# Optimization experiments

Hardware: AMD Instinct MI355X
Metric: run time of the kernel (lower is better)

Reference implementation:

```python
import jax, jax.numpy as jnp
import numpy as np


def setup_inputs() -> dict:
    key = jax.random.key(0)
    kx, kw = jax.random.split(key)
    x = jax.random.normal(kx, (32, 2048, 256), dtype=jnp.float32)
    W = jax.random.normal(kw, (1024, 256), dtype=jnp.float32)  # codebook [K, D]
    return {"x": x, "W": W}


def reference(x, W):
    D = W.shape[1]
    flat = x.reshape(-1, D)  # [N, D]
    # Squared Euclidean distances [N, K]; argmin is identical to cdist argmin.
    d2 = (
        jnp.sum(flat * flat, axis=1, keepdims=True)
        - 2.0 * (flat @ W.T)
        + jnp.sum(W * W, axis=1)
    )
    idx = jnp.argmin(d2, axis=1)  # [N]
    quant = W[idx].reshape(x.shape)  # direct gather == one-hot @ W
    # Straight-through estimator
    quantized = x + jax.lax.stop_gradient(quant - x)
    e_latent = jnp.mean((jax.lax.stop_gradient(quantized) - x) ** 2)
    q_latent = jnp.mean((quantized - jax.lax.stop_gradient(x)) ** 2)
    commitment_cost = 0.25
    loss = q_latent + commitment_cost * e_latent
    return quantized, loss, idx[:, None]
```

## Files before the change

### kernel.cpp

```cpp
#include <hip/hip_runtime.h>


#define NROWS    65536
#define DDIM     256
#define KCODES   1024
#define DEXT     512
#define ND_TOTAL 16777216

typedef __attribute__((ext_vector_type(8))) short bf16x8;
typedef __attribute__((ext_vector_type(4))) float floatx4;

__device__ __forceinline__ unsigned short f2bf(float f) {
    unsigned int u = __float_as_uint(f);
    return (unsigned short)((u + 0x7FFFu + ((u >> 16) & 1u)) >> 16);
}
__device__ __forceinline__ float bf2f(unsigned short h) {
    return __uint_as_float((unsigned int)h << 16);
}
__device__ __forceinline__ void split4(float4 v, ushort4* hi, ushort4* lo) {
    unsigned short hx = f2bf(v.x), hy = f2bf(v.y), hz = f2bf(v.z), hw = f2bf(v.w);
    *hi = make_ushort4(hx, hy, hz, hw);
    *lo = make_ushort4(f2bf(v.x - bf2f(hx)), f2bf(v.y - bf2f(hy)),
                       f2bf(v.z - bf2f(hz)), f2bf(v.w - bf2f(hw)));
}
__device__ __forceinline__ void async_copy16(void* lds, const void* g) {
    __builtin_amdgcn_global_load_lds(
        (const __attribute__((address_space(1))) unsigned int*)g,
        (__attribute__((address_space(3))) unsigned int*)lds, 16, 0, 0);
}

__device__ __forceinline__ void merge2(float& v1, int& k1, float& v2, int& k2,
                                       float o1, int ok1, float o2, int ok2) {
    bool aw = (v1 < o1) || (v1 == o1 && k1 < ok1);
    float ca = aw ? v2 : v1; int kca = aw ? k2 : k1;
    float cb = aw ? o1 : o2; int kcb = aw ? ok1 : ok2;
    float nv1 = aw ? v1 : o1; int nk1 = aw ? k1 : ok1;
    bool cw = (ca < cb) || (ca == cb && kca < kcb);
    v1 = nv1; k1 = nk1;
    v2 = cw ? ca : cb; k2 = cw ? kca : kcb;
}

__global__ __launch_bounds__(256) void vq_prepw(
    const float* __restrict__ W, unsigned short* __restrict__ What,
    float* __restrict__ w2, float* __restrict__ w2m,
    float* __restrict__ lossws, unsigned* __restrict__ ticket)
{
    int k = blockIdx.x * 256 + threadIdx.x;
    if (k == 0) { lossws[0] = 0.0f; ticket[0] = 0u; }
    const float4* wr = (const float4*)(W + (size_t)k * DDIM);
    unsigned short* hrow = What + (size_t)k * DEXT;
    float s = 0.0f;
    for (int i = 0; i < 64; ++i) {
        float4 v = wr[i];
        s = fmaf(v.x, v.x, s); s = fmaf(v.y, v.y, s);
        s = fmaf(v.z, v.z, s); s = fmaf(v.w, v.w, s);
        ushort4 hv, lv;
        split4(v, &hv, &lv);
        *(ushort4*)(hrow + i * 4) = hv;
        *(ushort4*)(hrow + 256 + i * 4) = lv;
    }
    w2[k] = s;
    w2m[k] = s - 256.0f;
}

__global__ __launch_bounds__(256, 2) void vq_main(
    unsigned short* Xhat, const unsigned short* __restrict__ What,
    const float* __restrict__ x, const float* __restrict__ W,
    const float* __restrict__ w2, const float* __restrict__ w2m,
    float* qout, float* lossws, unsigned* ticket, float* loss_out, float* idx_out)
{
    __shared__ __align__(16) unsigned short smem[2 * 16384];
    __shared__ float Wm[KCODES];

    int*   rk1   = (int*)smem;
    int*   rk2   = rk1 + 256;
    int*   candk = rk2 + 256;
    float* resc  = (float*)(candk + 512);
    int*   fink  = (int*)(resc + 512);

    const int tid  = threadIdx.x;
    const int wave = tid >> 6, lane = tid & 63;
    const int quad = lane >> 4, l15 = lane & 15;
    const int wr = wave >> 1, wc = wave & 1;
    const int row0 = blockIdx.x * 128;

    #pragma unroll
    for (int t = 0; t < 4; ++t) Wm[t * 256 + tid] = w2m[t * 256 + tid];

    #pragma unroll 4
    for (int it = 0; it < 32; ++it) {
        int gid = it * 256 + tid;
        int row = gid >> 6, qq = gid & 63;
        float4 v = ((const float4*)(x + (size_t)(row0 + row) * DDIM))[qq];
        ushort4 hv, lv;
        split4(v, &hv, &lv);
        unsigned short* r = Xhat + (size_t)(row0 + row) * DEXT;
        *(ushort4*)(r + qq * 4) = hv;
        *(ushort4*)(r + 256 + qq * 4) = lv;
    }
    __syncthreads();

    float s1[16], s2[16];
    #pragma unroll
    for (int s = 0; s < 16; ++s) { s1[s] = 3.0e38f; s2[s] = 3.0e38f; }

    const int r0 = tid >> 2, p0 = tid & 3;
    const int psw = (p0 ^ ((r0 >> 1) & 3)) << 3;
    const int quadS8 = (quad ^ ((l15 >> 1) & 3)) << 3;
    const unsigned short* Abase = Xhat + (size_t)row0 * DEXT + (size_t)r0 * DEXT + psw;
    const unsigned short* Bbase = What + (size_t)r0 * DEXT + psw;

    auto STAGE = [&](int q) {
        const int ct = q >> 3, dc = (q & 7) << 5;
        unsigned short* L = smem + (q & 1) * 16384 + tid * 8;
        const unsigned short* An = Abase + dc;
        const unsigned short* Bn = Bbase + (size_t)ct * 128 * DEXT + dc;
        async_copy16(L,          An);
        async_copy16(L + 2048,   An + 64 * DEXT);
        async_copy16(L + 4096,   An + 256);
        async_copy16(L + 6144,   An + 64 * DEXT + 256);
        async_copy16(L + 8192,   Bn);
        async_copy16(L + 10240,  Bn + 64 * DEXT);
        async_copy16(L + 12288,  Bn + 256);
        async_copy16(L + 14336,  Bn + 64 * DEXT + 256);
    };

    STAGE(0);

    floatx4 acc[4][4];
    #pragma unroll
    for (int i = 0; i < 4; ++i)
        #pragma unroll
        for (int j = 0; j < 4; ++j) acc[i][j] = (floatx4){0.f, 0.f, 0.f, 0.f};

    #pragma unroll 1
    for (int q = 0; q < 64; ++q) {
        asm volatile("s_waitcnt vmcnt(0)" ::: "memory");
        __builtin_amdgcn_s_barrier();
        asm volatile("" ::: "memory");
        if (q + 1 < 64) STAGE(q + 1);

        const unsigned short* Sb = smem + (q & 1) * 16384;
        bf16x8 a0[4], a1[4];
        #pragma unroll
        for (int i = 0; i < 4; ++i) {
            const int ro = (wr * 64 + i * 16 + l15) * 32 + quadS8;
            a0[i] = *(const bf16x8*)(Sb + ro);
            a1[i] = *(const bf16x8*)(Sb + 4096 + ro);
        }
        #pragma unroll
        for (int j = 0; j < 4; ++j) {
            const int ro = (wc * 64 + j * 16 + l15) * 32 + quadS8;
            bf16x8 b0 = *(const bf16x8*)(Sb + 8192 + ro);
            bf16x8 b1 = *(const bf16x8*)(Sb + 12288 + ro);
            __builtin_amdgcn_s_setprio(1);
            #pragma unroll
            for (int i = 0; i < 4; ++i) {
                acc[i][j] = __builtin_amdgcn_mfma_f32_16x16x32_bf16(a0[i], b0, acc[i][j], 0, 0, 0);
                acc[i][j] = __builtin_amdgcn_mfma_f32_16x16x32_bf16(a1[i], b1, acc[i][j], 0, 0, 0);
                acc[i][j] = __builtin_amdgcn_mfma_f32_16x16x32_bf16(a0[i], b1, acc[i][j], 0, 0, 0);
                acc[i][j] = __builtin_amdgcn_mfma_f32_16x16x32_bf16(a1[i], b0, acc[i][j], 0, 0, 0);
            }
            __builtin_amdgcn_s_setprio(0);
        }

        if ((q & 7) == 7) {
            const int ctf = q >> 3;
            #pragma unroll
            for (int j = 0; j < 4; ++j) {
                int cc = ctf * 128 + wc * 64 + j * 16 + l15;
                float wm = Wm[cc];
                unsigned pay = (unsigned)((j << 3) | ctf);
                #pragma unroll
                for (int i = 0; i < 4; ++i)
                    #pragma unroll
                    for (int r = 0; r < 4; ++r) {
                        float v = fmaf(-2.0f, acc[i][j][r], wm);
                        float pf = __uint_as_float((__float_as_uint(v) & 0xFFFFFFE0u) | pay);
                        int s = i * 4 + r;
                        float t = fminf(s1[s], pf);
                        s2[s] = fminf(s2[s], fmaxf(s1[s], pf));
                        s1[s] = t;
                    }
            }
            #pragma unroll
            for (int i = 0; i < 4; ++i)
                #pragma unroll
                for (int j = 0; j < 4; ++j) acc[i][j] = (floatx4){0.f, 0.f, 0.f, 0.f};
        }
    }

    float v1[16], v2[16];
    int k1[16], k2[16];
    #pragma unroll
    for (int s = 0; s < 16; ++s) {
        unsigned u1 = __float_as_uint(s1[s]) & 31u;
        unsigned u2 = __float_as_uint(s2[s]) & 31u;
        v1[s] = s1[s]; v2[s] = s2[s];
        k1[s] = (int)(u1 & 7u) * 128 + wc * 64 + (int)(u1 >> 3) * 16 + l15;
        k2[s] = (int)(u2 & 7u) * 128 + wc * 64 + (int)(u2 >> 3) * 16 + l15;
    }
    #pragma unroll
    for (int m = 1; m < 16; m <<= 1) {
        #pragma unroll
        for (int s = 0; s < 16; ++s) {
            float o1 = __shfl_xor(v1[s], m, 64);
            int  ok1 = __shfl_xor(k1[s], m, 64);
            float o2 = __shfl_xor(v2[s], m, 64);
            int  ok2 = __shfl_xor(k2[s], m, 64);
            merge2(v1[s], k1[s], v2[s], k2[s], o1, ok1, o2, ok2);
        }
    }
    if (l15 == 0) {
        #pragma unroll
        for (int s = 0; s < 16; ++s) {
            int row = wr * 64 + (s >> 2) * 16 + quad * 4 + (s & 3);
            rk1[wc * 128 + row] = k1[s];
            rk2[wc * 128 + row] = k2[s];
        }
    }
    __syncthreads();
    if (tid < 128) {
        candk[tid * 4 + 0] = rk1[tid];
        candk[tid * 4 + 1] = rk2[tid];
        candk[tid * 4 + 2] = rk1[128 + tid];
        candk[tid * 4 + 3] = rk2[128 + tid];
    }
    __syncthreads();
    #pragma unroll
    for (int j2 = 0; j2 < 2; ++j2) {
        int job = tid + j2 * 256;
        int r = job >> 2, cn = job & 3;
        int k = candk[r * 4 + cn];
        const float4* xr  = (const float4*)(x + (size_t)(row0 + r) * DDIM);
        const float4* wrp = (const float4*)(W + (size_t)k * DDIM);
        float dot = 0.0f;
        #pragma unroll 8
        for (int i = 0; i < 64; ++i) {
            float4 va = xr[i], vb = wrp[i];
            dot = fmaf(va.x, vb.x, dot); dot = fmaf(va.y, vb.y, dot);
            dot = fmaf(va.z, vb.z, dot); dot = fmaf(va.w, vb.w, dot);
        }
        resc[r * 4 + cn] = fmaf(-2.0f, dot, w2[k]);
    }
    __syncthreads();
    if (tid < 128) {
        float bd = resc[tid * 4 + 0];
        int   bk = candk[tid * 4 + 0];
        #pragma unroll
        for (int cn = 1; cn < 4; ++cn) {
            float d = resc[tid * 4 + cn];
            int   k = candk[tid * 4 + cn];
            if (d < bd || (d == bd && k < bk)) { bd = d; bk = k; }
        }
        fink[tid] = bk;
        idx_out[row0 + tid] = (float)bk;
    }
    __syncthreads();

    const int c4 = tid & 63, rsub = tid >> 6;
    float lsum = 0.0f;
    for (int it2 = 0; it2 < 32; ++it2) {
        int r = it2 * 4 + rsub;
        int k = fink[r];
        float4 wv = ((const float4*)(W + (size_t)k * DDIM))[c4];
        float4 xv = ((const float4*)(x + (size_t)(row0 + r) * DDIM))[c4];
        ((float4*)(qout + (size_t)(row0 + r) * DDIM))[c4] = wv;
        float dx = wv.x - xv.x, dy = wv.y - xv.y;
        float dz = wv.z - xv.z, dw = wv.w - xv.w;
        lsum = fmaf(dx, dx, lsum); lsum = fmaf(dy, dy, lsum);
        lsum = fmaf(dz, dz, lsum); lsum = fmaf(dw, dw, lsum);
    }
    #pragma unroll
    for (int off = 32; off > 0; off >>= 1) lsum += __shfl_down(lsum, off, 64);
    if (lane == 0) atomicAdd(lossws, lsum);

    __syncthreads();
    if (tid == 0) {
        __threadfence();
        unsigned old = atomicAdd(ticket, 1u);
        if (old == 511u) {
            float total = atomicAdd(lossws, 0.0f);
            loss_out[0] = 1.25f * total / (float)ND_TOTAL;
        }
    }
}

extern "C" void kernel_launch(void* const* d_in, const int* in_sizes, int n_in,
                              void* d_out, int out_size, void* d_ws, size_t ws_size,
                              hipStream_t stream) {
    const float* x = (const float*)d_in[0];
    const float* W = (const float*)d_in[1];
    float* out = (float*)d_out;
    unsigned short* Xhat = (unsigned short*)d_out;
    unsigned short* What = (unsigned short*)d_ws;
    float* w2     = (float*)((char*)d_ws + (1 << 20));
    float* w2m    = w2 + 1024;
    float* lossws = w2 + 2048;
    unsigned* ticket = (unsigned*)(w2 + 2049);
    float* loss_out = out + (size_t)ND_TOTAL;
    float* idx_out  = out + (size_t)ND_TOTAL + 1;

    vq_prepw<<<4, 256, 0, stream>>>(W, What, w2, w2m, lossws, ticket);
    vq_main<<<512, 256, 0, stream>>>(Xhat, What, x, W, w2, w2m, out,
                                     lossws, ticket, loss_out, idx_out);
}
```

Measured before the change: 335.7 us.

## Halve block row tile to 64, drop lo*lo MFMA term, rank top-4 candidates

```diff
diff --git a/kernel.cpp b/kernel.cpp
--- a/kernel.cpp
+++ b/kernel.cpp
@@ -63,32 +63,34 @@
     w2m[k] = s - 256.0f;
 }
 
-__global__ __launch_bounds__(256, 2) void vq_main(
+__global__ __launch_bounds__(256, 3) void vq_main(
     unsigned short* Xhat, const unsigned short* __restrict__ What,
     const float* __restrict__ x, const float* __restrict__ W,
     const float* __restrict__ w2, const float* __restrict__ w2m,
     float* qout, float* lossws, unsigned* ticket, float* loss_out, float* idx_out)
 {
-    __shared__ __align__(16) unsigned short smem[2 * 16384];
+    __shared__ __align__(16) unsigned short smem[2 * 12288];
     __shared__ float Wm[KCODES];
 
-    int*   rk1   = (int*)smem;
+    float* rv1   = (float*)smem;
+    float* rv2   = rv1 + 256;
+    int*   rk1   = (int*)(rv2 + 256);
     int*   rk2   = rk1 + 256;
     int*   candk = rk2 + 256;
-    float* resc  = (float*)(candk + 512);
-    int*   fink  = (int*)(resc + 512);
+    float* resc  = (float*)(candk + 256);
+    int*   fink  = (int*)(resc + 256);
 
     const int tid  = threadIdx.x;
     const int wave = tid >> 6, lane = tid & 63;
     const int quad = lane >> 4, l15 = lane & 15;
-    const int wr = wave >> 1, wc = wave & 1;
-    const int row0 = blockIdx.x * 128;
+    const int wc = wave;
+    const int row0 = blockIdx.x * 64;
 
     #pragma unroll
     for (int t = 0; t < 4; ++t) Wm[t * 256 + tid] = w2m[t * 256 + tid];
 
     #pragma unroll 4
-    for (int it = 0; it < 32; ++it) {
+    for (int it = 0; it < 16; ++it) {
         int gid = it * 256 + tid;
         int row = gid >> 6, qq = gid & 63;
         float4 v = ((const float4*)(x + (size_t)(row0 + row) * DDIM))[qq];
@@ -112,26 +114,24 @@
 
     auto STAGE = [&](int q) {
         const int ct = q >> 3, dc = (q & 7) << 5;
-        unsigned short* L = smem + (q & 1) * 16384 + tid * 8;
+        unsigned short* L = smem + (q & 1) * 12288 + tid * 8;
         const unsigned short* An = Abase + dc;
         const unsigned short* Bn = Bbase + (size_t)ct * 128 * DEXT + dc;
         async_copy16(L,          An);
-        async_copy16(L + 2048,   An + 64 * DEXT);
-        async_copy16(L + 4096,   An + 256);
-        async_copy16(L + 6144,   An + 64 * DEXT + 256);
-        async_copy16(L + 8192,   Bn);
-        async_copy16(L + 10240,  Bn + 64 * DEXT);
-        async_copy16(L + 12288,  Bn + 256);
-        async_copy16(L + 14336,  Bn + 64 * DEXT + 256);
+        async_copy16(L + 2048,   An + 256);
+        async_copy16(L + 4096,   Bn);
+        async_copy16(L + 6144,   Bn + 64 * DEXT);
+        async_copy16(L + 8192,   Bn + 256);
+        async_copy16(L + 10240,  Bn + 64 * DEXT + 256);
     };
 
     STAGE(0);
 
-    floatx4 acc[4][4];
+    floatx4 acc[4][2];
     #pragma unroll
     for (int i = 0; i < 4; ++i)
         #pragma unroll
-        for (int j = 0; j < 4; ++j) acc[i][j] = (floatx4){0.f, 0.f, 0.f, 0.f};
+        for (int j = 0; j < 2; ++j) acc[i][j] = (floatx4){0.f, 0.f, 0.f, 0.f};
 
     #pragma unroll 1
     for (int q = 0; q < 64; ++q) {
@@ -140,24 +140,23 @@
         asm volatile("" ::: "memory");
         if (q + 1 < 64) STAGE(q + 1);
 
-        const unsigned short* Sb = smem + (q & 1) * 16384;
+        const unsigned short* Sb = smem + (q & 1) * 12288;
         bf16x8 a0[4], a1[4];
         #pragma unroll
         for (int i = 0; i < 4; ++i) {
-            const int ro = (wr * 64 + i * 16 + l15) * 32 + quadS8;
+            const int ro = (i * 16 + l15) * 32 + quadS8;
             a0[i] = *(const bf16x8*)(Sb + ro);
-            a1[i] = *(const bf16x8*)(Sb + 4096 + ro);
-        }
-        #pragma unroll
-        for (int j = 0; j < 4; ++j) {
-            const int ro = (wc * 64 + j * 16 + l15) * 32 + quadS8;
-            bf16x8 b0 = *(const bf16x8*)(Sb + 8192 + ro);
-            bf16x8 b1 = *(const bf16x8*)(Sb + 12288 + ro);
+            a1[i] = *(const bf16x8*)(Sb + 2048 + ro);
+        }
+        #pragma unroll
+        for (int j = 0; j < 2; ++j) {
+            const int ro = (wc * 32 + j * 16 + l15) * 32 + quadS8;
+            bf16x8 b0 = *(const bf16x8*)(Sb + 4096 + ro);
+            bf16x8 b1 = *(const bf16x8*)(Sb + 8192 + ro);
             __builtin_amdgcn_s_setprio(1);
             #pragma unroll
             for (int i = 0; i < 4; ++i) {
                 acc[i][j] = __builtin_amdgcn_mfma_f32_16x16x32_bf16(a0[i], b0, acc[i][j], 0, 0, 0);
-                acc[i][j] = __builtin_amdgcn_mfma_f32_16x16x32_bf16(a1[i], b1, acc[i][j], 0, 0, 0);
                 acc[i][j] = __builtin_amdgcn_mfma_f32_16x16x32_bf16(a0[i], b1, acc[i][j], 0, 0, 0);
                 acc[i][j] = __builtin_amdgcn_mfma_f32_16x16x32_bf16(a1[i], b0, acc[i][j], 0, 0, 0);
             }
@@ -167,8 +166,8 @@
         if ((q & 7) == 7) {
             const int ctf = q >> 3;
             #pragma unroll
-            for (int j = 0; j < 4; ++j) {
-                int cc = ctf * 128 + wc * 64 + j * 16 + l15;
+            for (int j = 0; j < 2; ++j) {
+                int cc = ctf * 128 + wc * 32 + j * 16 + l15;
                 float wm = Wm[cc];
                 unsigned pay = (unsigned)((j << 3) | ctf);
                 #pragma unroll
@@ -176,7 +175,7 @@
                     #pragma unroll
                     for (int r = 0; r < 4; ++r) {
                         float v = fmaf(-2.0f, acc[i][j][r], wm);
-                        float pf = __uint_as_float((__float_as_uint(v) & 0xFFFFFFE0u) | pay);
+                        float pf = __uint_as_float((__float_as_uint(v) & 0xFFFFFFF0u) | pay);
                         int s = i * 4 + r;
                         float t = fminf(s1[s], pf);
                         s2[s] = fminf(s2[s], fmaxf(s1[s], pf));
@@ -186,7 +185,7 @@
             #pragma unroll
             for (int i = 0; i < 4; ++i)
                 #pragma unroll
-                for (int j = 0; j < 4; ++j) acc[i][j] = (floatx4){0.f, 0.f, 0.f, 0.f};
+                for (int j = 0; j < 2; ++j) acc[i][j] = (floatx4){0.f, 0.f, 0.f, 0.f};
         }
     }
 
@@ -194,11 +193,11 @@
     int k1[16], k2[16];
     #pragma unroll
     for (int s = 0; s < 16; ++s) {
-        unsigned u1 = __float_as_uint(s1[s]) & 31u;
-        unsigned u2 = __float_as_uint(s2[s]) & 31u;
+        unsigned u1 = __float_as_uint(s1[s]) & 15u;
+        unsigned u2 = __float_as_uint(s2[s]) & 15u;
         v1[s] = s1[s]; v2[s] = s2[s];
-        k1[s] = (int)(u1 & 7u) * 128 + wc * 64 + (int)(u1 >> 3) * 16 + l15;
-        k2[s] = (int)(u2 & 7u) * 128 + wc * 64 + (int)(u2 >> 3) * 16 + l15;
+        k1[s] = (int)(u1 & 7u) * 128 + wc * 32 + (int)(u1 >> 3) * 16 + l15;
+        k2[s] = (int)(u2 & 7u) * 128 + wc * 32 + (int)(u2 >> 3) * 16 + l15;
     }
     #pragma unroll
     for (int m = 1; m < 16; m <<= 1) {
@@ -214,37 +213,48 @@
     if (l15 == 0) {
         #pragma unroll
         for (int s = 0; s < 16; ++s) {
-            int row = wr * 64 + (s >> 2) * 16 + quad * 4 + (s & 3);
-            rk1[wc * 128 + row] = k1[s];
-            rk2[wc * 128 + row] = k2[s];
-        }
-    }
-    __syncthreads();
-    if (tid < 128) {
-        candk[tid * 4 + 0] = rk1[tid];
-        candk[tid * 4 + 1] = rk2[tid];
-        candk[tid * 4 + 2] = rk1[128 + tid];
-        candk[tid * 4 + 3] = rk2[128 + tid];
-    }
-    __syncthreads();
-    #pragma unroll
-    for (int j2 = 0; j2 < 2; ++j2) {
-        int job = tid + j2 * 256;
-        int r = job >> 2, cn = job & 3;
-        int k = candk[r * 4 + cn];
+            int row = (s >> 2) * 16 + quad * 4 + (s & 3);
+            rv1[wc * 64 + row] = v1[s]; rk1[wc * 64 + row] = k1[s];
+            rv2[wc * 64 + row] = v2[s]; rk2[wc * 64 + row] = k2[s];
+        }
+    }
+    __syncthreads();
+    if (tid < 64) {
+        float pv[8]; int pk[8];
+        #pragma unroll
+        for (int h = 0; h < 4; ++h) {
+            pv[h * 2 + 0] = rv1[h * 64 + tid]; pk[h * 2 + 0] = rk1[h * 64 + tid];
+            pv[h * 2 + 1] = rv2[h * 64 + tid]; pk[h * 2 + 1] = rk2[h * 64 + tid];
+        }
+        #pragma unroll
+        for (int a = 0; a < 8; ++a) {
+            int rank = 0;
+            #pragma unroll
+            for (int b = 0; b < 8; ++b)
+                rank += (pv[b] < pv[a] || (pv[b] == pv[a] && pk[b] < pk[a])) ? 1 : 0;
+            if (rank == 0) candk[tid * 4 + 0] = pk[a];
+            if (rank == 1) candk[tid * 4 + 1] = pk[a];
+            if (rank == 2) candk[tid * 4 + 2] = pk[a];
+            if (rank == 3) candk[tid * 4 + 3] = pk[a];
+        }
+    }
+    __syncthreads();
+    {
+        int r = tid >> 2;
+        int k = candk[tid];
         const float4* xr  = (const float4*)(x + (size_t)(row0 + r) * DDIM);
         const float4* wrp = (const float4*)(W + (size_t)k * DDIM);
         float dot = 0.0f;
-        #pragma unroll 8
+        #pragma unroll 16
         for (int i = 0; i < 64; ++i) {
             float4 va = xr[i], vb = wrp[i];
             dot = fmaf(va.x, vb.x, dot); dot = fmaf(va.y, vb.y, dot);
             dot = fmaf(va.z, vb.z, dot); dot = fmaf(va.w, vb.w, dot);
         }
-        resc[r * 4 + cn] = fmaf(-2.0f, dot, w2[k]);
-    }
-    __syncthreads();
-    if (tid < 128) {
+        resc[tid] = fmaf(-2.0f, dot, w2[k]);
+    }
+    __syncthreads();
+    if (tid < 64) {
         float bd = resc[tid * 4 + 0];
         int   bk = candk[tid * 4 + 0];
         #pragma unroll
@@ -260,7 +270,7 @@
 
     const int c4 = tid & 63, rsub = tid >> 6;
     float lsum = 0.0f;
-    for (int it2 = 0; it2 < 32; ++it2) {
+    for (int it2 = 0; it2 < 16; ++it2) {
         int r = it2 * 4 + rsub;
         int k = fink[r];
         float4 wv = ((const float4*)(W + (size_t)k * DDIM))[c4];
@@ -279,7 +289,7 @@
     if (tid == 0) {
         __threadfence();
         unsigned old = atomicAdd(ticket, 1u);
-        if (old == 511u) {
+        if (old == 1023u) {
             float total = atomicAdd(lossws, 0.0f);
             loss_out[0] = 1.25f * total / (float)ND_TOTAL;
         }
@@ -302,6 +312,6 @@
     float* idx_out  = out + (size_t)ND_TOTAL + 1;
 
     vq_prepw<<<4, 256, 0, stream>>>(W, What, w2, w2m, lossws, ticket);
-    vq_main<<<512, 256, 0, stream>>>(Xhat, What, x, W, w2, w2m, out,
-                                     lossws, ticket, loss_out, idx_out);
-}
+    vq_main<<<1024, 256, 0, stream>>>(Xhat, What, x, W, w2, w2m, out,
+                                      lossws, ticket, loss_out, idx_out);
+}
```

Result: slower. 408.4 us (+21.7%).

## Drop lo*lo MFMA term, interleave hi/lo layout, widen block to 512 threads

Applied to the files above, without the earlier changes.

```diff
diff --git a/kernel.cpp b/kernel.cpp
--- a/kernel.cpp
+++ b/kernel.cpp
@@ -56,47 +56,49 @@
         s = fmaf(v.z, v.z, s); s = fmaf(v.w, v.w, s);
         ushort4 hv, lv;
         split4(v, &hv, &lv);
-        *(ushort4*)(hrow + i * 4) = hv;
-        *(ushort4*)(hrow + 256 + i * 4) = lv;
+        int h = i >> 2, pos = i & 3;
+        *(ushort4*)(hrow + h * 32 + pos * 4) = hv;
+        *(ushort4*)(hrow + h * 32 + 16 + pos * 4) = lv;
     }
     w2[k] = s;
     w2m[k] = s - 256.0f;
 }
 
-__global__ __launch_bounds__(256, 2) void vq_main(
+__global__ __launch_bounds__(512, 4) void vq_main(
     unsigned short* Xhat, const unsigned short* __restrict__ What,
     const float* __restrict__ x, const float* __restrict__ W,
     const float* __restrict__ w2, const float* __restrict__ w2m,
     float* qout, float* lossws, unsigned* ticket, float* loss_out, float* idx_out)
 {
-    __shared__ __align__(16) unsigned short smem[2 * 16384];
+    __shared__ __align__(16) unsigned short smem[2 * 12288];
     __shared__ float Wm[KCODES];
 
     int*   rk1   = (int*)smem;
-    int*   rk2   = rk1 + 256;
-    int*   candk = rk2 + 256;
-    float* resc  = (float*)(candk + 512);
-    int*   fink  = (int*)(resc + 512);
+    int*   rk2   = rk1 + 512;
+    int*   candk = rk2 + 512;
+    float* resc  = (float*)(candk + 1024);
+    int*   fink  = (int*)(resc + 1024);
 
     const int tid  = threadIdx.x;
     const int wave = tid >> 6, lane = tid & 63;
     const int quad = lane >> 4, l15 = lane & 15;
-    const int wr = wave >> 1, wc = wave & 1;
+    const int wr = wave >> 2, wc = wave & 3;
     const int row0 = blockIdx.x * 128;
 
-    #pragma unroll
-    for (int t = 0; t < 4; ++t) Wm[t * 256 + tid] = w2m[t * 256 + tid];
+    Wm[tid] = w2m[tid];
+    Wm[512 + tid] = w2m[512 + tid];
 
     #pragma unroll 4
-    for (int it = 0; it < 32; ++it) {
-        int gid = it * 256 + tid;
+    for (int it = 0; it < 16; ++it) {
+        int gid = it * 512 + tid;
         int row = gid >> 6, qq = gid & 63;
         float4 v = ((const float4*)(x + (size_t)(row0 + row) * DDIM))[qq];
         ushort4 hv, lv;
         split4(v, &hv, &lv);
         unsigned short* r = Xhat + (size_t)(row0 + row) * DEXT;
-        *(ushort4*)(r + qq * 4) = hv;
-        *(ushort4*)(r + 256 + qq * 4) = lv;
+        int h = qq >> 2, pos = qq & 3;
+        *(ushort4*)(r + h * 32 + pos * 4) = hv;
+        *(ushort4*)(r + h * 32 + 16 + pos * 4) = lv;
     }
     __syncthreads();
 
@@ -111,18 +113,13 @@
     const unsigned short* Bbase = What + (size_t)r0 * DEXT + psw;
 
     auto STAGE = [&](int q) {
-        const int ct = q >> 3, dc = (q & 7) << 5;
-        unsigned short* L = smem + (q & 1) * 16384 + tid * 8;
+        const int ct = q >> 4, dc = (q & 15) << 5;
+        unsigned short* L = smem + (q & 1) * 12288 + tid * 8;
         const unsigned short* An = Abase + dc;
-        const unsigned short* Bn = Bbase + (size_t)ct * 128 * DEXT + dc;
-        async_copy16(L,          An);
-        async_copy16(L + 2048,   An + 64 * DEXT);
-        async_copy16(L + 4096,   An + 256);
-        async_copy16(L + 6144,   An + 64 * DEXT + 256);
-        async_copy16(L + 8192,   Bn);
-        async_copy16(L + 10240,  Bn + 64 * DEXT);
-        async_copy16(L + 12288,  Bn + 256);
-        async_copy16(L + 14336,  Bn + 64 * DEXT + 256);
+        const unsigned short* Bn = Bbase + (size_t)ct * 256 * DEXT + dc;
+        async_copy16(L,        An);
+        async_copy16(L + 4096, Bn);
+        async_copy16(L + 8192, Bn + 128 * DEXT);
     };
 
     STAGE(0);
@@ -140,43 +137,41 @@
         asm volatile("" ::: "memory");
         if (q + 1 < 64) STAGE(q + 1);
 
-        const unsigned short* Sb = smem + (q & 1) * 16384;
-        bf16x8 a0[4], a1[4];
+        const unsigned short* Sb = smem + (q & 1) * 12288;
+        bf16x8 a[4];
         #pragma unroll
         for (int i = 0; i < 4; ++i) {
-            const int ro = (wr * 64 + i * 16 + l15) * 32 + quadS8;
-            a0[i] = *(const bf16x8*)(Sb + ro);
-            a1[i] = *(const bf16x8*)(Sb + 4096 + ro);
+            const int r = wr * 64 + i * 16 + l15;
+            a[i] = *(const bf16x8*)(Sb + r * 32 + quadS8);
         }
         #pragma unroll
         for (int j = 0; j < 4; ++j) {
-            const int ro = (wc * 64 + j * 16 + l15) * 32 + quadS8;
-            bf16x8 b0 = *(const bf16x8*)(Sb + 8192 + ro);
-            bf16x8 b1 = *(const bf16x8*)(Sb + 12288 + ro);
+            const int rb = wc * 64 + j * 16 + l15;
+            const int bo = 4096 + rb * 32 + quadS8;
+            bf16x8 bn = *(const bf16x8*)(Sb + bo);
+            bf16x8 bs = *(const bf16x8*)(Sb + (bo ^ 16));
             __builtin_amdgcn_s_setprio(1);
             #pragma unroll
             for (int i = 0; i < 4; ++i) {
-                acc[i][j] = __builtin_amdgcn_mfma_f32_16x16x32_bf16(a0[i], b0, acc[i][j], 0, 0, 0);
-                acc[i][j] = __builtin_amdgcn_mfma_f32_16x16x32_bf16(a1[i], b1, acc[i][j], 0, 0, 0);
-                acc[i][j] = __builtin_amdgcn_mfma_f32_16x16x32_bf16(a0[i], b1, acc[i][j], 0, 0, 0);
-                acc[i][j] = __builtin_amdgcn_mfma_f32_16x16x32_bf16(a1[i], b0, acc[i][j], 0, 0, 0);
+                acc[i][j] = __builtin_amdgcn_mfma_f32_16x16x32_bf16(a[i], bn, acc[i][j], 0, 0, 0);
+                acc[i][j] = __builtin_amdgcn_mfma_f32_16x16x32_bf16(a[i], bs, acc[i][j], 0, 0, 0);
             }
             __builtin_amdgcn_s_setprio(0);
         }
 
-        if ((q & 7) == 7) {
-            const int ctf = q >> 3;
+        if ((q & 15) == 15) {
+            const int ctf = q >> 4;
             #pragma unroll
             for (int j = 0; j < 4; ++j) {
-                int cc = ctf * 128 + wc * 64 + j * 16 + l15;
+                int cc = ctf * 256 + wc * 64 + j * 16 + l15;
                 float wm = Wm[cc];
-                unsigned pay = (unsigned)((j << 3) | ctf);
+                unsigned pay = (unsigned)((j << 2) | ctf);
                 #pragma unroll
                 for (int i = 0; i < 4; ++i)
                     #pragma unroll
                     for (int r = 0; r < 4; ++r) {
                         float v = fmaf(-2.0f, acc[i][j][r], wm);
-                        float pf = __uint_as_float((__float_as_uint(v) & 0xFFFFFFE0u) | pay);
+                        float pf = __uint_as_float((__float_as_uint(v) & 0xFFFFFFF0u) | pay);
                         int s = i * 4 + r;
                         float t = fminf(s1[s], pf);
                         s2[s] = fminf(s2[s], fmaxf(s1[s], pf));
@@ -194,11 +189,11 @@
     int k1[16], k2[16];
     #pragma unroll
     for (int s = 0; s < 16; ++s) {
-        unsigned u1 = __float_as_uint(s1[s]) & 31u;
-        unsigned u2 = __float_as_uint(s2[s]) & 31u;
+        unsigned u1 = __float_as_uint(s1[s]) & 15u;
+        unsigned u2 = __float_as_uint(s2[s]) & 15u;
         v1[s] = s1[s]; v2[s] = s2[s];
-        k1[s] = (int)(u1 & 7u) * 128 + wc * 64 + (int)(u1 >> 3) * 16 + l15;
-        k2[s] = (int)(u2 & 7u) * 128 + wc * 64 + (int)(u2 >> 3) * 16 + l15;
+        k1[s] = (int)(u1 & 3u) * 256 + wc * 64 + (int)(u1 >> 2) * 16 + l15;
+        k2[s] = (int)(u2 & 3u) * 256 + wc * 64 + (int)(u2 >> 2) * 16 + l15;
     }
     #pragma unroll
     for (int m = 1; m < 16; m <<= 1) {
@@ -221,17 +216,18 @@
     }
     __syncthreads();
     if (tid < 128) {
-        candk[tid * 4 + 0] = rk1[tid];
-        candk[tid * 4 + 1] = rk2[tid];
-        candk[tid * 4 + 2] = rk1[128 + tid];
-        candk[tid * 4 + 3] = rk2[128 + tid];
+        #pragma unroll
+        for (int h = 0; h < 4; ++h) {
+            candk[tid * 8 + h * 2 + 0] = rk1[h * 128 + tid];
+            candk[tid * 8 + h * 2 + 1] = rk2[h * 128 + tid];
+        }
     }
     __syncthreads();
     #pragma unroll
     for (int j2 = 0; j2 < 2; ++j2) {
-        int job = tid + j2 * 256;
-        int r = job >> 2, cn = job & 3;
-        int k = candk[r * 4 + cn];
+        int job = tid + j2 * 512;
+        int r = job >> 3, cn = job & 7;
+        int k = candk[r * 8 + cn];
         const float4* xr  = (const float4*)(x + (size_t)(row0 + r) * DDIM);
         const float4* wrp = (const float4*)(W + (size_t)k * DDIM);
         float dot = 0.0f;
@@ -241,16 +237,16 @@
             dot = fmaf(va.x, vb.x, dot); dot = fmaf(va.y, vb.y, dot);
             dot = fmaf(va.z, vb.z, dot); dot = fmaf(va.w, vb.w, dot);
         }
-        resc[r * 4 + cn] = fmaf(-2.0f, dot, w2[k]);
+        resc[r * 8 + cn] = fmaf(-2.0f, dot, w2[k]);
     }
     __syncthreads();
     if (tid < 128) {
-        float bd = resc[tid * 4 + 0];
-        int   bk = candk[tid * 4 + 0];
-        #pragma unroll
-        for (int cn = 1; cn < 4; ++cn) {
-            float d = resc[tid * 4 + cn];
-            int   k = candk[tid * 4 + cn];
+        float bd = resc[tid * 8 + 0];
+        int   bk = candk[tid * 8 + 0];
+        #pragma unroll
+        for (int cn = 1; cn < 8; ++cn) {
+            float d = resc[tid * 8 + cn];
+            int   k = candk[tid * 8 + cn];
             if (d < bd || (d == bd && k < bk)) { bd = d; bk = k; }
         }
         fink[tid] = bk;
@@ -260,8 +256,8 @@
 
     const int c4 = tid & 63, rsub = tid >> 6;
     float lsum = 0.0f;
-    for (int it2 = 0; it2 < 32; ++it2) {
-        int r = it2 * 4 + rsub;
+    for (int it2 = 0; it2 < 16; ++it2) {
+        int r = it2 * 8 + rsub;
         int k = fink[r];
         float4 wv = ((const float4*)(W + (size_t)k * DDIM))[c4];
         float4 xv = ((const float4*)(x + (size_t)(row0 + r) * DDIM))[c4];
@@ -302,6 +298,6 @@
     float* idx_out  = out + (size_t)ND_TOTAL + 1;
 
     vq_prepw<<<4, 256, 0, stream>>>(W, What, w2, w2m, lossws, ticket);
-    vq_main<<<512, 256, 0, stream>>>(Xhat, What, x, W, w2, w2m, out,
+    vq_main<<<512, 512, 0, stream>>>(Xhat, What, x, W, w2, w2m, out,
                                      lossws, ticket, loss_out, idx_out);
 }
```

New measurement: 450.0 us. +34.0%, slower.
